# Kernel optimization log

Measured on AMD Instinct MI355X. Metric: run time of the kernel, lower is better.

The kernel has to match this reference:

```python
import jax, jax.numpy as jnp
import numpy as np

# Dimensions (match init_kwargs / input_specs)
N = 50000      # num_nodes
R = 16         # num_relations
B = 8          # num_bases
DIN = 128      # indim
DOUT = 128     # outdim
NNZ = 1_600_000  # nonzeros in block-sparse relational adjacency A (N x R*N)


def setup_inputs() -> dict:
    key = jax.random.key(0)
    k0, k1, k2, k3, k4, k5 = jax.random.split(key, 6)
    X = jax.random.normal(k0, (N, DIN), dtype=jnp.float32)
    # COO representation of sparse A: rows in [0, N), cols in [0, R*N)
    A_rows = jax.random.randint(k1, (NNZ,), 0, N, dtype=jnp.int64)
    A_cols = jax.random.randint(k2, (NNZ,), 0, R * N, dtype=jnp.int64)
    A_vals = jax.random.uniform(k3, (NNZ,), dtype=jnp.float32)
    # Basis-decomposed relation weights (xavier-ish scale)
    weight_F = jax.random.normal(k4, (B, DIN, DOUT), dtype=jnp.float32) * 0.05
    weight_F_comp = jax.random.normal(k5, (R, B), dtype=jnp.float32) * 0.3
    return {"X": X, "A_rows": A_rows, "A_cols": A_cols, "A_vals": A_vals,
            "weight_F": weight_F, "weight_F_comp": weight_F_comp}


def reference(X, A_rows, A_cols, A_vals, weight_F, weight_F_comp):
    # Basis decomposition: per-relation weights W_F[r] = sum_b comp[r,b] * basis[b]
    W_F = jnp.einsum('rb,bij->rij', weight_F_comp, weight_F)          # (R, DIN, DOUT)
    # Per-relation feature transform: X @ W_F[r] for all r
    FW_F = jnp.einsum('nj,rjk->rnk', X, W_F)                          # (R, N, DOUT)
    FW_F = FW_F.reshape(R * N, DOUT)                                  # (R*N, DOUT)
    # Sparse-dense matmul A @ FW_F via gather + weighted segment-sum
    gathered = A_vals[:, None] * FW_F[A_cols]                          # (NNZ, DOUT)
    AFW_F = jax.ops.segment_sum(gathered, A_rows, num_segments=N)     # (N, DOUT)
    return AFW_F
```

## Files before the change

kernel.cpp:

```cpp
#include <hip/hip_runtime.h>

typedef unsigned int   uint32;
typedef unsigned short ushort16;

#define NN       50000
#define RR       16
#define BB       8
#define DIN      128
#define DOUT     128
#define K2       1024
#define NNZ_C    1600000
#define NBUCK    196
#define EPB      4096
#define NBLK_E   391

typedef short  short8  __attribute__((ext_vector_type(8)));
typedef float  floatx4 __attribute__((ext_vector_type(4)));

__device__ __forceinline__ ushort16 f2bf(float f) {
    uint32 u = __float_as_uint(f);
    u += 0x7fffu + ((u >> 16) & 1u);
    return (ushort16)(u >> 16);
}

__device__ __forceinline__ float bf2f(ushort16 h) {
    return __uint_as_float(((uint32)h) << 16);
}

__device__ __forceinline__ uint32 pack_bf16(float a, float b) {
    uint32 ua = __float_as_uint(a) + 0x8000u;
    uint32 ub = __float_as_uint(b) + 0x8000u;
    return __builtin_amdgcn_perm(ub, ua, 0x07060302);
}

__device__ __forceinline__ void gload16(const void* g, void* l) {
    __builtin_amdgcn_global_load_lds(
        (const __attribute__((address_space(1))) uint32*)g,
        (__attribute__((address_space(3))) uint32*)l, 16, 0, 0);
}

__global__ void build_bst_kernel(const float* __restrict__ basis,
                                 ushort16* __restrict__ Bst) {
    int idx  = blockIdx.x * 256 + threadIdx.x;
    int jout = idx >> 10;
    int bk   = idx & 1023;
    Bst[idx] = f2bf(basis[(size_t)bk * DOUT + jout]);
}

__global__ void cvt_x_kernel(const float* __restrict__ X,
                             uint32* __restrict__ XD) {
    int d = blockIdx.x * 256 + threadIdx.x;
    float2 f = *(const float2*)(X + (size_t)d * 2);
    XD[d] = pack_bf16(f.x, f.y);
}

__global__ void histB_kernel(const int* __restrict__ rows,
                             int* __restrict__ counts) {
    __shared__ int h[NBUCK];
    int tid = threadIdx.x;
    if (tid < NBUCK) h[tid] = 0;
    __syncthreads();
    int base_e = blockIdx.x * EPB;
#pragma unroll
    for (int it = 0; it < 16; ++it) {
        int e = base_e + it * 256 + tid;
        if (e < NNZ_C) atomicAdd(&h[rows[e] >> 8], 1);
    }
    __syncthreads();
    if (tid < NBUCK && h[tid]) atomicAdd(&counts[tid], h[tid]);
}

__global__ void scanB_kernel(const int* __restrict__ counts,
                             int* __restrict__ bucket_start,
                             int* __restrict__ cursor) {
    __shared__ int tmp[256];
    int tid = threadIdx.x;
    int v = (tid < NBUCK) ? counts[tid] : 0;
    tmp[tid] = v;
    __syncthreads();
#pragma unroll
    for (int off = 1; off < 256; off <<= 1) {
        int t = (tid >= off) ? tmp[tid - off] : 0;
        __syncthreads();
        tmp[tid] += t;
        __syncthreads();
    }
    if (tid < NBUCK) {
        bucket_start[tid + 1] = tmp[tid];
        cursor[tid] = tmp[tid] - v;
        if (tid == 0) bucket_start[0] = 0;
    }
}

__global__ __launch_bounds__(256) void scatterB_kernel(
        const int* __restrict__ rows,
        const int* __restrict__ cols,
        const float* __restrict__ vals,
        int* __restrict__ cursor,
        uint2* __restrict__ es2) {
    __shared__ int h[NBUCK], gbase[NBUCK], lcur[NBUCK];
    int tid = threadIdx.x;
    if (tid < NBUCK) { h[tid] = 0; lcur[tid] = 0; }
    __syncthreads();

    int    rowv[16];
    uint32 pkx[16];
    float  vv[16];
    int base_e = blockIdx.x * EPB;
#pragma unroll
    for (int it = 0; it < 16; ++it) {
        int e = base_e + it * 256 + tid;
        if (e < NNZ_C) {
            int row = rows[e];
            int col = cols[e];
            int r   = (int)((uint32)col / (uint32)NN);
            int c   = col - r * NN;
            rowv[it] = row;
            pkx[it]  = (uint32)c | ((uint32)(((row & 255) << 4) | r) << 16);
            vv[it]   = vals[e];
            atomicAdd(&h[row >> 8], 1);
        } else rowv[it] = -1;
    }
    __syncthreads();
    if (tid < NBUCK && h[tid] > 0)
        gbase[tid] = atomicAdd(&cursor[tid], h[tid]);
    __syncthreads();
#pragma unroll
    for (int it = 0; it < 16; ++it) {
        if (rowv[it] >= 0) {
            int b   = rowv[it] >> 8;
            int pos = gbase[b] + atomicAdd(&lcur[b], 1);
            es2[pos] = make_uint2(pkx[it], __float_as_uint(vv[it]));
        }
    }
}

__global__ __launch_bounds__(256) void sortB_kernel(
        const uint2* __restrict__ es2,
        const int* __restrict__ bucket_start,
        uint2* __restrict__ es,
        int* __restrict__ ks) {
    __shared__ int h[4096];
    __shared__ int cur[4096];
    __shared__ int tmp[256];
    int b    = blockIdx.x;
    int tid  = threadIdx.x;
    int base = bucket_start[b];
    int n    = bucket_start[b + 1] - base;

#pragma unroll
    for (int j = 0; j < 16; ++j) h[j * 256 + tid] = 0;
    __syncthreads();
    for (int i = tid; i < n; i += 256) {
        uint2 p = es2[base + i];
        atomicAdd(&h[(p.x >> 16) & 0xfffu], 1);
    }
    __syncthreads();

    int run = 0;
    int loc[16];
#pragma unroll
    for (int j = 0; j < 16; ++j) {
        int c = h[tid * 16 + j];
        loc[j] = run;
        run += c;
    }
    tmp[tid] = run;
    __syncthreads();
#pragma unroll
    for (int off = 1; off < 256; off <<= 1) {
        int t = (tid >= off) ? tmp[tid - off] : 0;
        __syncthreads();
        tmp[tid] += t;
        __syncthreads();
    }
    int excl_t = tmp[tid] - run;
#pragma unroll
    for (int j = 0; j < 16; ++j) {
        int idx = tid * 16 + j;
        int st  = loc[j] + excl_t;
        cur[idx] = st;
        ks[b * 4096 + idx] = base + st;
    }
    __syncthreads();

    for (int i = tid; i < n; i += 256) {
        uint2 p  = es2[base + i];
        int   kl = (p.x >> 16) & 0xfffu;
        int  pos = atomicAdd(&cur[kl], 1);
        es[base + pos] = make_uint2(p.x & 0xffffu, p.y);
    }
}

__global__ __launch_bounds__(256) void zc_build_kernel(
        const uint2* __restrict__ es,
        const int* __restrict__ ks,
        const uint32* __restrict__ XD,
        const float* __restrict__ comp,
        uint32* __restrict__ ZD) {
    __shared__ float comp_l[128];
    int tid = threadIdx.x;
    if (tid < 128) comp_l[tid] = comp[tid];
    __syncthreads();

    int row  = blockIdx.x * 4 + (tid >> 6);
    int lane = tid & 63;

    int s = (lane < 17) ? ks[row * 16 + lane] : 0;
    int beg     = __shfl(s, 0);
    int end_row = __shfl(s, 16);

    float zb0[8] = {0.f,0.f,0.f,0.f,0.f,0.f,0.f,0.f};
    float zb1[8] = {0.f,0.f,0.f,0.f,0.f,0.f,0.f,0.f};
    float a0 = 0.f, a1 = 0.f;
    int r_cur = 0;
    int nxt = __shfl(s, 1);

    uint2 p0 = (beg + 0 < end_row) ? es[beg + 0] : make_uint2(0u, 0u);
    uint2 p1 = (beg + 1 < end_row) ? es[beg + 1] : make_uint2(0u, 0u);
    uint2 p2 = (beg + 2 < end_row) ? es[beg + 2] : make_uint2(0u, 0u);
    uint2 p3 = (beg + 3 < end_row) ? es[beg + 3] : make_uint2(0u, 0u);

#define FLUSH                                                             \
    { _Pragma("unroll")                                                   \
      for (int b = 0; b < 8; ++b) {                                       \
          float cb = comp_l[r_cur * 8 + b];                               \
          zb0[b] += cb * a0; zb1[b] += cb * a1;                           \
      }                                                                   \
      a0 = a1 = 0.f; r_cur++;                                             \
      nxt = (r_cur < 16) ? __shfl(s, r_cur + 1) : 0x7fffffff; }

#define CONSUME(P, XV, IDX)                                               \
    { int idx_ = (IDX);                                                   \
      while (idx_ >= nxt && r_cur < 16) FLUSH                             \
      if (idx_ < end_row) {                                               \
          float v_ = __uint_as_float((P).y);                              \
          a0 += v_ * bf2f((ushort16)((XV) & 0xffffu));                    \
          a1 += v_ * bf2f((ushort16)((XV) >> 16));                        \
      } }

    for (int e = beg; e < end_row; e += 4) {
        uint2 n0 = (e + 4 < end_row) ? es[e + 4] : make_uint2(0u, 0u);
        uint2 n1 = (e + 5 < end_row) ? es[e + 5] : make_uint2(0u, 0u);
        uint2 n2 = (e + 6 < end_row) ? es[e + 6] : make_uint2(0u, 0u);
        uint2 n3 = (e + 7 < end_row) ? es[e + 7] : make_uint2(0u, 0u);
        uint32 x0 = XD[((p0.x & 0xffffu) << 6) + lane];
        uint32 x1 = XD[((p1.x & 0xffffu) << 6) + lane];
        uint32 x2 = XD[((p2.x & 0xffffu) << 6) + lane];
        uint32 x3 = XD[((p3.x & 0xffffu) << 6) + lane];
        CONSUME(p0, x0, e + 0)
        CONSUME(p1, x1, e + 1)
        CONSUME(p2, x2, e + 2)
        CONSUME(p3, x3, e + 3)
        p0 = n0; p1 = n1; p2 = n2; p3 = n3;
    }
    while (r_cur < 16) FLUSH

#pragma unroll
    for (int b = 0; b < 8; ++b)
        ZD[(size_t)row * 512 + b * 64 + lane] = pack_bf16(zb0[b], zb1[b]);
#undef CONSUME
#undef FLUSH
}

__global__ __launch_bounds__(256) void gemm_out_kernel(
        const ushort16* __restrict__ Zc,
        const ushort16* __restrict__ Bst,
        float* __restrict__ out) {
    __shared__ __align__(16) char lds[32768];
    char* Al = lds;
    char* Bl = lds + 16384;

    const int tid  = threadIdx.x;
    const int wave = tid >> 6;
    const int lane = tid & 63;
    const int m    = lane & 15;
    const int half = lane >> 4;
    const int wr   = wave >> 1;
    const int wc   = wave & 1;
    const size_t arow0 = (size_t)blockIdx.x * 128;

    floatx4 acc[16] = {};

    for (int slab = 0; slab < 16; ++slab) {
        const int k0 = slab * 64;
#pragma unroll
        for (int rd = 0; rd < 4; ++rd) {
            int s   = rd * 256 + wave * 64 + lane;
            int row = s >> 3;
            int kc  = (s & 7) ^ (row & 7);
            size_t ldsoff = (size_t)(rd * 256 + wave * 64) * 16;
            gload16(Zc  + ((arow0 + row) << 10) + k0 + (kc << 3), Al + ldsoff);
            gload16(Bst + ((size_t)row << 10)   + k0 + (kc << 3), Bl + ldsoff);
        }
        __syncthreads();

#pragma unroll
        for (int c = 0; c < 2; ++c) {
            short8 a[4], bfr[4];
#pragma unroll
            for (int mt = 0; mt < 4; ++mt) {
                int row = wr * 64 + mt * 16 + m;
                int p   = row * 8 + ((c * 4 + half) ^ (m & 7));
                a[mt] = *(const short8*)(Al + p * 16);
            }
#pragma unroll
            for (int nt = 0; nt < 4; ++nt) {
                int rowb = wc * 64 + nt * 16 + m;
                int p    = rowb * 8 + ((c * 4 + half) ^ (m & 7));
                bfr[nt] = *(const short8*)(Bl + p * 16);
            }
#pragma unroll
            for (int mt = 0; mt < 4; ++mt)
#pragma unroll
                for (int nt = 0; nt < 4; ++nt)
                    acc[mt * 4 + nt] = __builtin_amdgcn_mfma_f32_16x16x32_bf16(
                        a[mt], bfr[nt], acc[mt * 4 + nt], 0, 0, 0);
        }
        __syncthreads();
    }

#pragma unroll
    for (int mt = 0; mt < 4; ++mt) {
#pragma unroll
        for (int reg = 0; reg < 4; ++reg) {
            int grow = (int)arow0 + wr * 64 + mt * 16 + half * 4 + reg;
            if (grow < NN) {
#pragma unroll
                for (int nt = 0; nt < 4; ++nt)
                    out[(size_t)grow * DOUT + wc * 64 + nt * 16 + m] =
                        acc[mt * 4 + nt][reg];
            }
        }
    }
}

extern "C" void kernel_launch(void* const* d_in, const int* in_sizes, int n_in,
                              void* d_out, int out_size, void* d_ws, size_t ws_size,
                              hipStream_t stream) {
    const float* X      = (const float*)d_in[0];
    const int*   A_rows = (const int*)d_in[1];
    const int*   A_cols = (const int*)d_in[2];
    const float* A_vals = (const float*)d_in[3];
    const float* basis  = (const float*)d_in[4];
    const float* comp   = (const float*)d_in[5];
    float* out = (float*)d_out;

    char* ws = (char*)d_ws;
    ushort16* Bst          = (ushort16*)(ws + 0);
    uint32*   XD           = (uint32*)(ws + 524288);
    int*      ks           = (int*)(ws + 13324288);
    uint2*    es           = (uint2*)(ws + 16535552);
    int*      bucket_start = (int*)(ws + 29335552);
    int*      counts       = (int*)(ws + 29336576);
    int*      cursor       = (int*)(ws + 29337600);
    uint2*    es2          = (uint2*)(ws + 29339648);
    ushort16* Zc           = (ushort16*)(ws + 42139648);
    uint32*   ZD           = (uint32*)Zc;

    hipMemsetAsync(counts, 0, NBUCK * sizeof(int), stream);

    build_bst_kernel<<<512, 256, 0, stream>>>(basis, Bst);
    cvt_x_kernel<<<12500, 256, 0, stream>>>(X, XD);

    histB_kernel<<<NBLK_E, 256, 0, stream>>>(A_rows, counts);
    scanB_kernel<<<1, 256, 0, stream>>>(counts, bucket_start, cursor);
    scatterB_kernel<<<NBLK_E, 256, 0, stream>>>(A_rows, A_cols, A_vals,
                                                cursor, es2);
    sortB_kernel<<<NBUCK, 256, 0, stream>>>(es2, bucket_start, es, ks);

    zc_build_kernel<<<12500, 256, 0, stream>>>(es, ks, XD, comp, ZD);

    gemm_out_kernel<<<(NN + 127) / 128, 256, 0, stream>>>(Zc, Bst, out);
}
```

Before: 277.1 us.

## Embed relation id in edges and deepen gather pipeline in zc_build

The bucketing kernel now stores each edge's relation index in the upper bits of its packed record. The zc_build kernel then folds per-relation accumulators by comparing that id, instead of walking segment boundaries with shuffles and while-loops. Edge metadata is made wave-uniform through readfirstlane, and the gather loop becomes a two-stage software pipeline eight records deep. Accumulation uses packed float2 vectors and comp is read with float4 LDS loads. The aim is to cut scalar and branch overhead and hide more gather latency, at the cost of higher register pressure.

New measurement: 260.5 us. 1.06x faster.

```diff
diff --git a/kernel.cpp b/kernel.cpp
--- a/kernel.cpp
+++ b/kernel.cpp
@@ -16,6 +16,7 @@
 
 typedef short  short8  __attribute__((ext_vector_type(8)));
 typedef float  floatx4 __attribute__((ext_vector_type(4)));
+typedef float  float2v __attribute__((ext_vector_type(2)));
 
 __device__ __forceinline__ ushort16 f2bf(float f) {
     uint32 u = __float_as_uint(f);
@@ -188,7 +189,8 @@
         uint2 p  = es2[base + i];
         int   kl = (p.x >> 16) & 0xfffu;
         int  pos = atomicAdd(&cur[kl], 1);
-        es[base + pos] = make_uint2(p.x & 0xffffu, p.y);
+        es[base + pos] = make_uint2((p.x & 0xffffu) | ((uint32)(kl & 15) << 16),
+                                    p.y);
     }
 }
 
@@ -198,69 +200,119 @@
         const uint32* __restrict__ XD,
         const float* __restrict__ comp,
         uint32* __restrict__ ZD) {
-    __shared__ float comp_l[128];
+    __shared__ __align__(16) float comp_l[128];
     int tid = threadIdx.x;
     if (tid < 128) comp_l[tid] = comp[tid];
     __syncthreads();
 
-    int row  = blockIdx.x * 4 + (tid >> 6);
-    int lane = tid & 63;
-
-    int s = (lane < 17) ? ks[row * 16 + lane] : 0;
-    int beg     = __shfl(s, 0);
-    int end_row = __shfl(s, 16);
-
-    float zb0[8] = {0.f,0.f,0.f,0.f,0.f,0.f,0.f,0.f};
-    float zb1[8] = {0.f,0.f,0.f,0.f,0.f,0.f,0.f,0.f};
-    float a0 = 0.f, a1 = 0.f;
-    int r_cur = 0;
-    int nxt = __shfl(s, 1);
-
-    uint2 p0 = (beg + 0 < end_row) ? es[beg + 0] : make_uint2(0u, 0u);
-    uint2 p1 = (beg + 1 < end_row) ? es[beg + 1] : make_uint2(0u, 0u);
-    uint2 p2 = (beg + 2 < end_row) ? es[beg + 2] : make_uint2(0u, 0u);
-    uint2 p3 = (beg + 3 < end_row) ? es[beg + 3] : make_uint2(0u, 0u);
-
-#define FLUSH                                                             \
-    { _Pragma("unroll")                                                   \
-      for (int b = 0; b < 8; ++b) {                                       \
-          float cb = comp_l[r_cur * 8 + b];                               \
-          zb0[b] += cb * a0; zb1[b] += cb * a1;                           \
-      }                                                                   \
-      a0 = a1 = 0.f; r_cur++;                                             \
-      nxt = (r_cur < 16) ? __shfl(s, r_cur + 1) : 0x7fffffff; }
-
-#define CONSUME(P, XV, IDX)                                               \
-    { int idx_ = (IDX);                                                   \
-      while (idx_ >= nxt && r_cur < 16) FLUSH                             \
-      if (idx_ < end_row) {                                               \
-          float v_ = __uint_as_float((P).y);                              \
-          a0 += v_ * bf2f((ushort16)((XV) & 0xffffu));                    \
-          a1 += v_ * bf2f((ushort16)((XV) >> 16));                        \
-      } }
-
-    for (int e = beg; e < end_row; e += 4) {
-        uint2 n0 = (e + 4 < end_row) ? es[e + 4] : make_uint2(0u, 0u);
-        uint2 n1 = (e + 5 < end_row) ? es[e + 5] : make_uint2(0u, 0u);
-        uint2 n2 = (e + 6 < end_row) ? es[e + 6] : make_uint2(0u, 0u);
-        uint2 n3 = (e + 7 < end_row) ? es[e + 7] : make_uint2(0u, 0u);
-        uint32 x0 = XD[((p0.x & 0xffffu) << 6) + lane];
-        uint32 x1 = XD[((p1.x & 0xffffu) << 6) + lane];
-        uint32 x2 = XD[((p2.x & 0xffffu) << 6) + lane];
-        uint32 x3 = XD[((p3.x & 0xffffu) << 6) + lane];
-        CONSUME(p0, x0, e + 0)
-        CONSUME(p1, x1, e + 1)
-        CONSUME(p2, x2, e + 2)
-        CONSUME(p3, x3, e + 3)
-        p0 = n0; p1 = n1; p2 = n2; p3 = n3;
-    }
-    while (r_cur < 16) FLUSH
+    const int row  = __builtin_amdgcn_readfirstlane(blockIdx.x * 4 + (tid >> 6));
+    const int lane = tid & 63;
+
+    int beg = __builtin_amdgcn_readfirstlane(ks[row * 16]);
+    int end = __builtin_amdgcn_readfirstlane(ks[row * 16 + 16]);
+
+    float2v zb[8];
+#pragma unroll
+    for (int b = 0; b < 8; ++b) zb[b] = (float2v){0.f, 0.f};
+
+    if (beg < end) {
+        const int endm1 = end - 1;
+        float2v a = (float2v){0.f, 0.f};
+
+#define LREC(C, R, V, IDX)                                                 \
+        { int i_ = (IDX) < endm1 ? (IDX) : endm1;                          \
+          uint2 pz_ = es[i_];                                              \
+          uint32 px_ = __builtin_amdgcn_readfirstlane(pz_.x);              \
+          V = __uint_as_float(__builtin_amdgcn_readfirstlane(pz_.y));      \
+          C = (int)(px_ & 0xffffu); R = (int)(px_ >> 16); }
+
+#define LX(X, C)  X = XD[((size_t)(C) << 6) + lane];
+
+#define FOLD                                                               \
+        { float4 c0_ = *(const float4*)&comp_l[r_cur * 8];                 \
+          float4 c1_ = *(const float4*)&comp_l[r_cur * 8 + 4];             \
+          zb[0] += c0_.x * a; zb[1] += c0_.y * a;                          \
+          zb[2] += c0_.z * a; zb[3] += c0_.w * a;                          \
+          zb[4] += c1_.x * a; zb[5] += c1_.y * a;                          \
+          zb[6] += c1_.z * a; zb[7] += c1_.w * a; }
+
+#define CONS(R, V, X, K)                                                   \
+        if (e + (K) < end) {                                               \
+            if ((R) != r_cur) {                                            \
+                FOLD                                                       \
+                a = (float2v){0.f, 0.f};                                   \
+                r_cur = (R);                                               \
+            }                                                              \
+            float2v xf_;                                                   \
+            xf_.x = __uint_as_float((X) << 16);                            \
+            xf_.y = __uint_as_float((X) & 0xffff0000u);                    \
+            a += (V) * xf_;                                                \
+        }
+
+        int   cA0, cA1, cA2, cA3, rA0, rA1, rA2, rA3;
+        int   cB0, cB1, cB2, cB3, rB0, rB1, rB2, rB3;
+        float vA0, vA1, vA2, vA3, vB0, vB1, vB2, vB3;
+        uint32 xA0, xA1, xA2, xA3;
+
+        LREC(cA0, rA0, vA0, beg + 0)
+        LREC(cA1, rA1, vA1, beg + 1)
+        LREC(cA2, rA2, vA2, beg + 2)
+        LREC(cA3, rA3, vA3, beg + 3)
+        LREC(cB0, rB0, vB0, beg + 4)
+        LREC(cB1, rB1, vB1, beg + 5)
+        LREC(cB2, rB2, vB2, beg + 6)
+        LREC(cB3, rB3, vB3, beg + 7)
+        LX(xA0, cA0) LX(xA1, cA1) LX(xA2, cA2) LX(xA3, cA3)
+
+        int r_cur = rA0;
+
+        for (int e = beg; e < end; e += 8) {
+            uint32 xB0, xB1, xB2, xB3;
+            LX(xB0, cB0) LX(xB1, cB1) LX(xB2, cB2) LX(xB3, cB3)
+            int cC0, cC1, cC2, cC3, rC0, rC1, rC2, rC3;
+            float vC0, vC1, vC2, vC3;
+            LREC(cC0, rC0, vC0, e + 8)
+            LREC(cC1, rC1, vC1, e + 9)
+            LREC(cC2, rC2, vC2, e + 10)
+            LREC(cC3, rC3, vC3, e + 11)
+
+            CONS(rA0, vA0, xA0, 0)
+            CONS(rA1, vA1, xA1, 1)
+            CONS(rA2, vA2, xA2, 2)
+            CONS(rA3, vA3, xA3, 3)
+
+            uint32 xC0, xC1, xC2, xC3;
+            LX(xC0, cC0) LX(xC1, cC1) LX(xC2, cC2) LX(xC3, cC3)
+            int cD0, cD1, cD2, cD3, rD0, rD1, rD2, rD3;
+            float vD0, vD1, vD2, vD3;
+            LREC(cD0, rD0, vD0, e + 12)
+            LREC(cD1, rD1, vD1, e + 13)
+            LREC(cD2, rD2, vD2, e + 14)
+            LREC(cD3, rD3, vD3, e + 15)
+
+            CONS(rB0, vB0, xB0, 4)
+            CONS(rB1, vB1, xB1, 5)
+            CONS(rB2, vB2, xB2, 6)
+            CONS(rB3, vB3, xB3, 7)
+
+            cA0 = cC0; cA1 = cC1; cA2 = cC2; cA3 = cC3;
+            rA0 = rC0; rA1 = rC1; rA2 = rC2; rA3 = rC3;
+            vA0 = vC0; vA1 = vC1; vA2 = vC2; vA3 = vC3;
+            xA0 = xC0; xA1 = xC1; xA2 = xC2; xA3 = xC3;
+            cB0 = cD0; cB1 = cD1; cB2 = cD2; cB3 = cD3;
+            rB0 = rD0; rB1 = rD1; rB2 = rD2; rB3 = rD3;
+            vB0 = vD0; vB1 = vD1; vB2 = vD2; vB3 = vD3;
+        }
+        FOLD
+#undef CONS
+#undef FOLD
+#undef LX
+#undef LREC
+    }
 
 #pragma unroll
     for (int b = 0; b < 8; ++b)
-        ZD[(size_t)row * 512 + b * 64 + lane] = pack_bf16(zb0[b], zb1[b]);
-#undef CONSUME
-#undef FLUSH
+        ZD[(size_t)row * 512 + b * 64 + lane] = pack_bf16(zb[b].x, zb[b].y);
 }
 
 __global__ __launch_bounds__(256) void gemm_out_kernel(
```
